# Performance work log

Hardware: AMD Instinct MI355X
Metric: run time of the kernel (lower is better)

Reference implementation:

```python
import jax, jax.numpy as jnp
import numpy as np
from jax import lax

N = 16384
K = 16
EPS = 1e-5


def setup_inputs() -> dict:
    key = jax.random.key(0)
    ks = jax.random.split(key, 10)

    def w(k, shape):
        fan_in = shape[0]
        return jax.random.normal(k, shape, jnp.float32) / np.sqrt(fan_in)

    return {
        "pos": jax.random.normal(ks[0], (N, 3), jnp.float32),
        "normal": jax.random.normal(ks[1], (N, 3), jnp.float32),
        # conv1 mlp: Linear(9,64) -> GroupNorm(8,64) -> ReLU -> Linear(64,64)
        "W1a": w(ks[2], (9, 64)), "b1a": jnp.zeros((64,), jnp.float32),
        "g1": jnp.ones((64,), jnp.float32), "beta1": jnp.zeros((64,), jnp.float32),
        "W1b": w(ks[3], (64, 64)), "b1b": jnp.zeros((64,), jnp.float32),
        # conv2 mlp: Linear(67,64) -> GroupNorm(8,64) -> ReLU -> Linear(64,64)
        "W2a": w(ks[4], (67, 64)), "b2a": jnp.zeros((64,), jnp.float32),
        "g2": jnp.ones((64,), jnp.float32), "beta2": jnp.zeros((64,), jnp.float32),
        "W2b": w(ks[5], (64, 64)), "b2b": jnp.zeros((64,), jnp.float32),
        # conv3 mlp: Linear(67,128) -> GroupNorm(16,128) -> ReLU -> Linear(128,128)
        "W3a": w(ks[6], (67, 128)), "b3a": jnp.zeros((128,), jnp.float32),
        "g3": jnp.ones((128,), jnp.float32), "beta3": jnp.zeros((128,), jnp.float32),
        "W3b": w(ks[7], (128, 128)), "b3b": jnp.zeros((128,), jnp.float32),
    }


def knn_graph(pos, k):
    # [N,N] squared distances; loop=True -> self is included (distance 0).
    sq = jnp.sum(pos * pos, axis=1)
    d2 = sq[:, None] + sq[None, :] - 2.0 * (pos @ pos.T)
    _, nbr = lax.top_k(-d2, k)  # [N,k] neighbor (source) indices per target node
    return nbr


def group_norm(h, gamma, beta, groups):
    # h: [N,k,C]; normalize each group of channels per edge sample.
    n, k, c = h.shape
    hg = h.reshape(n, k, groups, c // groups)
    mu = hg.mean(axis=-1, keepdims=True)
    var = hg.var(axis=-1, keepdims=True)
    hg = (hg - mu) * lax.rsqrt(var + EPS)
    return hg.reshape(n, k, c) * gamma + beta


def pointnet_conv(x, pos, nbr, Wa, ba, gamma, beta, Wb, bb, groups):
    # message: concat(x_j, pos_j - pos_i), MLP per edge, max-aggregate over neighbors
    xj = x[nbr]                              # [N,k,C_in]
    rel = pos[nbr] - pos[:, None, :]         # [N,k,3]
    m = jnp.concatenate([xj, rel], axis=-1)  # [N,k,C_in+3]
    h = m @ Wa + ba
    h = jax.nn.relu(group_norm(h, gamma, beta, groups))
    h = h @ Wb + bb
    return jnp.max(h, axis=1)                # [N,C_out]


def reference(pos, normal, W1a, b1a, g1, beta1, W1b, b1b,
              W2a, b2a, g2, beta2, W2b, b2b,
              W3a, b3a, g3, beta3, W3b, b3b):
    nbr = knn_graph(pos, K)
    h = jnp.concatenate([pos, normal], axis=-1)  # [N,6]
    h1 = jax.nn.relu(pointnet_conv(h, pos, nbr, W1a, b1a, g1, beta1, W1b, b1b, 8))
    h2 = jax.nn.relu(pointnet_conv(h1, pos, nbr, W2a, b2a, g2, beta2, W2b, b2b, 8))
    h3 = jax.nn.relu(pointnet_conv(h2, pos, nbr, W3a, b3a, g3, beta3, W3b, b3b, 16))
    return (h1, h2, h3)
```

## Files before the change

### kernel.cpp

```cpp
#include <hip/hip_runtime.h>
#include <hip/hip_bf16.h>
#include <stdint.h>

typedef unsigned long long u64;
typedef unsigned int u32;
typedef __attribute__((ext_vector_type(8))) short bf16x8;
typedef __attribute__((ext_vector_type(8))) unsigned short u16x8;
typedef __attribute__((ext_vector_type(4))) float f32x4;

__device__ __forceinline__ float ldv(const void* p, size_t idx, int mode) {
  return mode ? __bfloat162float(((const __hip_bfloat16*)p)[idx])
              : ((const float*)p)[idx];
}
__device__ __forceinline__ void stv(void* p, size_t idx, int mode, float v) {
  if (mode) ((__hip_bfloat16*)p)[idx] = __float2bfloat16(v);
  else      ((float*)p)[idx] = v;
}
__device__ __forceinline__ unsigned short f2bfb(float f) {
  u32 u = __float_as_uint(f);
  u32 r = u + 0x7fffu + ((u >> 16) & 1u);
  return (unsigned short)(r >> 16);
}
__device__ __forceinline__ float bfb2f(unsigned short b) {
  return __uint_as_float((u32)b << 16);
}
__device__ __forceinline__ u64 shfl64(u64 v, int src) {
  int lo = __shfl((int)(u32)(v & 0xffffffffu), src, 64);
  int hi = __shfl((int)(u32)(v >> 32), src, 64);
  return ((u64)(u32)hi << 32) | (u32)lo;
}
__device__ __forceinline__ u64 shflxor64(u64 v, int m) {
  int lo = __shfl_xor((int)(u32)(v & 0xffffffffu), m, 64);
  int hi = __shfl_xor((int)(u32)(v >> 32), m, 64);
  return ((u64)(u32)hi << 32) | (u32)lo;
}
__device__ __forceinline__ u64 shfl64w16(u64 v, int src) {
  int lo = __shfl((int)(u32)(v & 0xffffffffu), src, 16);
  int hi = __shfl((int)(u32)(v >> 32), src, 16);
  return ((u64)(u32)hi << 32) | (u32)lo;
}

__device__ __forceinline__ u32 benc(float f) {
  u32 u = __float_as_uint(f);
  return (u & 0x80000000u) ? ~u : (u | 0x80000000u);
}
__device__ __forceinline__ float bdec(u32 k) {
  return (k & 0x80000000u) ? __uint_as_float(k ^ 0x80000000u)
                           : __uint_as_float(~k);
}

__global__ void PointNetSimple_61409442398998_kernel() {}

struct CvtEnt { const void* src; float* dst; int n; };
struct CvtArgs { CvtEnt e[12]; };
struct WEnt { const void* src; unsigned short* dst; int K, N, Kpad; };
struct WArgs { WEnt e[6]; };

#define GR 32
#define GR3 (GR*GR*GR)

__global__ void setup_kernel(const void* __restrict__ pos,
                             const void* __restrict__ nrm,
                             WArgs wa, CvtArgs ca,
                             int* __restrict__ flag,
                             float4* __restrict__ pos4,
                             float* __restrict__ h0,
                             int* __restrict__ counts, int n) {
  const unsigned short* u16p = (const unsigned short*)pos;
  int cnt = 0;
  for (int k = 0; k < 32; ++k) {
    int e = (u16p[k] >> 7) & 0xff;
    if (e >= 110 && e <= 140) cnt++;
  }
  const int mode = (cnt >= 26) ? 1 : 0;

  const int nprep = n >> 8;
  const int b = blockIdx.x;
  if (b < nprep) {
    int i = b * 256 + threadIdx.x;
    float x = ldv(pos, 3*(size_t)i+0, mode);
    float y = ldv(pos, 3*(size_t)i+1, mode);
    float z = ldv(pos, 3*(size_t)i+2, mode);
    pos4[i] = make_float4(x, y, z, x*x + y*y + z*z);
    h0[6*(size_t)i+0] = x; h0[6*(size_t)i+1] = y; h0[6*(size_t)i+2] = z;
    h0[6*(size_t)i+3] = ldv(nrm, 3*(size_t)i+0, mode);
    h0[6*(size_t)i+4] = ldv(nrm, 3*(size_t)i+1, mode);
    h0[6*(size_t)i+5] = ldv(nrm, 3*(size_t)i+2, mode);
    float bmn[3] = {x, y, z}, bmx[3] = {x, y, z};
#pragma unroll
    for (int m = 32; m; m >>= 1) {
#pragma unroll
      for (int k = 0; k < 3; ++k) {
        bmn[k] = fminf(bmn[k], __shfl_xor(bmn[k], m, 64));
        bmx[k] = fmaxf(bmx[k], __shfl_xor(bmx[k], m, 64));
      }
    }
    if ((threadIdx.x & 63) == 0) {
      u32* bb = (u32*)flag;
#pragma unroll
      for (int k = 0; k < 3; ++k) {
        atomicMin(&bb[4 + k], benc(bmn[k]));
        atomicMin(&bb[7 + k], benc(-bmx[k]));
      }
    }
  } else {
    int r = b - nprep;
    if (r < 6) {
      WEnt ent = wa.e[r];
      for (int t = threadIdx.x; t < ent.N * ent.Kpad; t += blockDim.x) {
        int nn = t / ent.Kpad;
        int k  = t - nn * ent.Kpad;
        float v = (k < ent.K) ? ldv(ent.src, (size_t)k * ent.N + nn, mode) : 0.0f;
        ent.dst[t] = f2bfb(v);
      }
      if (r == 0 && threadIdx.x == 0) flag[0] = mode;
    } else if (r == 6) {
      for (int t2 = 0; t2 < 12; ++t2) {
        CvtEnt ent = ca.e[t2];
        for (int t = threadIdx.x; t < ent.n; t += blockDim.x)
          ent.dst[t] = ldv(ent.src, t, mode);
      }
    } else {
      counts[(r - 7) * 256 + threadIdx.x] = 0;
    }
  }
}

template<int CAP>
__device__ __forceinline__ void knn_flush(u64* __restrict__ wbuf, int& cnt,
                                          u64& val, u64& t15, float& th,
                                          int lane) {
  u64 cand = (lane < cnt) ? wbuf[lane] : ~0ull;
#pragma unroll
  for (int k = 2; k <= CAP; k <<= 1) {
#pragma unroll
    for (int j = k >> 1; j > 0; j >>= 1) {
      u64 other = shflxor64(cand, j);
      bool up    = ((lane & k) == 0) || (k == CAP);
      bool lower = ((lane & j) == 0);
      bool keepMin = (up == lower);
      u64 mn = cand < other ? cand : other;
      u64 mx = cand < other ? other : cand;
      cand = keepMin ? mn : mx;
    }
  }
  u64 rev = shfl64w16(cand, 15 - (lane & 15));
  u64 lo = val < rev ? val : rev;
#pragma unroll
  for (int j = 8; j > 0; j >>= 1) {
    u64 other = shflxor64(lo, j);
    bool lower = ((lane & j) == 0);
    u64 mn = lo < other ? lo : other;
    u64 mx = lo < other ? other : lo;
    lo = lower ? mn : mx;
  }
  val = (lane < 16) ? lo : ~0ull;
  t15 = shfl64(val, 15);
  u32 thb = (u32)(t15 >> 32);
  th = (thb == 0xffffffffu) ? 3.4e38f : __uint_as_float(thb);
  cnt = 0;
}

__global__ __launch_bounds__(256) void hist_kernel(
    const float4* __restrict__ pos4, const u32* __restrict__ bbx,
    int* __restrict__ counts, int* __restrict__ cid, int n) {
  const int i = blockIdx.x * 256 + threadIdx.x;
  if (i >= n) return;
  const float mnx = bdec(bbx[0]), mny = bdec(bbx[1]), mnz = bdec(bbx[2]);
  const float ihx = (float)GR / fmaxf(-bdec(bbx[3]) - mnx, 1e-20f);
  const float ihy = (float)GR / fmaxf(-bdec(bbx[4]) - mny, 1e-20f);
  const float ihz = (float)GR / fmaxf(-bdec(bbx[5]) - mnz, 1e-20f);
  float4 p = pos4[i];
  int cx = min(GR - 1, max(0, (int)((p.x - mnx) * ihx)));
  int cy = min(GR - 1, max(0, (int)((p.y - mny) * ihy)));
  int cz = min(GR - 1, max(0, (int)((p.z - mnz) * ihz)));
  int lin = (cz * GR + cy) * GR + cx;
  cid[i] = lin;
  atomicAdd(&counts[lin], 1);
}

__global__ __launch_bounds__(1024) void scan_kernel(
    const int* __restrict__ counts, int* __restrict__ cellstart,
    int* __restrict__ cursor) {
  __shared__ int part[1024];
  const int t = threadIdx.x;
  int4 v[8];
  int s = 0;
#pragma unroll
  for (int k = 0; k < 8; ++k) {
    v[k] = ((const int4*)counts)[t*8 + k];
    s += v[k].x + v[k].y + v[k].z + v[k].w;
  }
  part[t] = s;
  __syncthreads();
  for (int d = 1; d < 1024; d <<= 1) {
    int x = (t >= d) ? part[t - d] : 0;
    __syncthreads();
    part[t] += x;
    __syncthreads();
  }
  int o = part[t] - s;
#pragma unroll
  for (int k = 0; k < 8; ++k) {
    int4 c;
    c.x = o; o += v[k].x;
    c.y = o; o += v[k].y;
    c.z = o; o += v[k].z;
    c.w = o; o += v[k].w;
    ((int4*)cellstart)[t*8 + k] = c;
    ((int4*)cursor)[t*8 + k] = c;
  }
  if (t == 1023) { cellstart[GR3] = o; cursor[GR3] = o; }
}

__global__ __launch_bounds__(256) void scatter_kernel(
    const float4* __restrict__ pos4, const int* __restrict__ cid,
    int* __restrict__ cursor, int* __restrict__ sidx,
    float4* __restrict__ spos4, int n) {
  const int i = blockIdx.x * 256 + threadIdx.x;
  if (i >= n) return;
  int dst = atomicAdd(&cursor[cid[i]], 1);
  spos4[dst] = pos4[i];
  sidx[dst]  = i;
}

#define KNN7_WPB 4
__global__ __launch_bounds__(256) void knn7_kernel(
    const float4* __restrict__ spos4,
    const int* __restrict__ sidx, const int* __restrict__ cellstart,
    const u32* __restrict__ bbx, int* __restrict__ nbr, int n) {
  __shared__ u64 buf[KNN7_WPB][72];
  const int tid = threadIdx.x, lane = tid & 63, w = tid >> 6;
  const int g = blockIdx.x * KNN7_WPB + w;
  u64* wbuf = &buf[w][0];
  const float4 pi = spos4[g];
  const int target = sidx[g];

  const float mnx = bdec(bbx[0]), mny = bdec(bbx[1]), mnz = bdec(bbx[2]);
  const float ex = fmaxf(-bdec(bbx[3]) - mnx, 1e-20f);
  const float ey = fmaxf(-bdec(bbx[4]) - mny, 1e-20f);
  const float ez = fmaxf(-bdec(bbx[5]) - mnz, 1e-20f);
  const float ihx = (float)GR / ex, ihy = (float)GR / ey, ihz = (float)GR / ez;
  const float hxf = ex * (1.0f / GR), hyf = ey * (1.0f / GR), hzf = ez * (1.0f / GR);
  const int cx = min(GR - 1, max(0, (int)((pi.x - mnx) * ihx)));
  const int cy = min(GR - 1, max(0, (int)((pi.y - mny) * ihy)));
  const int cz = min(GR - 1, max(0, (int)((pi.z - mnz) * ihz)));

  u64 val = ~0ull, t15 = ~0ull;
  float th = 3.4e38f;
  int cnt = 0;
  int myseen = 0;

  auto doFlush = [&]() {
    if (cnt <= 32) knn_flush<32>(wbuf, cnt, val, t15, th, lane);
    else           knn_flush<64>(wbuf, cnt, val, t15, th, lane);
  };

  auto procSeg = [&](int p0, int p1) {
#pragma unroll 2
    for (int t0 = p0; t0 < p1; t0 += 64) {
      int gi = t0 + lane;
      bool in = gi < p1;
      float4 a = spos4[in ? gi : (p1 - 1)];
      float d2 = (pi.w + a.w) - 2.0f*(pi.x*a.x + pi.y*a.y + pi.z*a.z);
      d2 = fmaxf(d2, 0.0f);
      bool pass = in && (d2 <= th);
      u64 bal = __ballot(pass);
      if (bal) {
        int pc = __popcll(bal);
        if (cnt + pc > 64) doFlush();
        u32 mb = __builtin_amdgcn_mbcnt_lo((u32)bal, 0u);
        mb = __builtin_amdgcn_mbcnt_hi((u32)(bal >> 32), mb);
        if (pass)
          wbuf[cnt + mb] = ((u64)__float_as_uint(d2) << 32) | (u32)sidx[gi];
        cnt += pc;
      }
    }
  };

  {
    const int oc = (cz * GR + cy) * GR + cx;
    const int oLo = cellstart[oc], oHi = cellstart[oc + 1];
    if (lane == 0) myseen += oHi - oLo;
    procSeg(oLo, oHi);
    if (cnt > 0) doFlush();
  }

  for (int r = 1; r < GR; ++r) {
    const int x0 = max(cx - r, 0), x1 = min(cx + r, GR - 1);
    const int d1 = 2*r + 1, d2i = 2*r - 1;
    const int nA = 2 * d1;
    const int nB = 2 * d2i;
    const int nC = 2 * d2i * d2i;
    const int S = nA + nB + nC;
    const u32 magic = 0xFFFFFFFFu / (u32)d2i + 1u;

    for (int b0 = 0; b0 < S; b0 += 64) {
      const int s = b0 + lane;
      int zc = 0, yc = 0, xa = 0, xb = -1;
      bool live = s < S;
      if (live) {
        if (s < nA) {
          int za = s >= d1;
          int dy = s - (za ? d1 : 0) - r;
          zc = cz + (za ? r : -r); yc = cy + dy; xa = x0; xb = x1;
        } else if (s < nA + nB) {
          int t = s - nA;
          int side = t >= d2i;
          int dz = t - (side ? d2i : 0) - (r - 1);
          zc = cz + dz; yc = cy + (side ? r : -r); xa = x0; xb = x1;
        } else {
          int t = s - nA - nB;
          int side = t & 1; t >>= 1;
          int dzi = (int)__umulhi((u32)t, magic);
          int dyi = t - dzi * d2i;
          zc = cz - r + 1 + dzi; yc = cy - r + 1 + dyi;
          int xcell = side ? cx + r : cx - r;
          xa = xcell; xb = xcell;
          live = ((unsigned)xcell < GR);
        }
        live = live && ((unsigned)zc < GR) && ((unsigned)yc < GR);
      }
      int lo = 0, hi = 0;
      if (live) {
        int base = (zc * GR + yc) * GR;
        lo = cellstart[base + xa];
        hi = cellstart[base + xb + 1];
        myseen += hi - lo;
      }
      u64 bal = __ballot(live && (hi > lo));
      while (bal) {
        int l = __builtin_ctzll(bal); bal &= bal - 1;
        int p0 = __shfl(lo, l, 64), p1 = __shfl(hi, l, 64);
        procSeg(p0, p1);
      }
    }

    int tot = myseen;
#pragma unroll
    for (int m = 32; m; m >>= 1) tot += __shfl_xor(tot, m, 64);
    if (tot >= n) break;
    float mind = 3.4e38f;
    if (cx - r > 0)      mind = fminf(mind, pi.x - (mnx + (float)(cx - r) * hxf));
    if (cx + r < GR - 1) mind = fminf(mind, (mnx + (float)(cx + r + 1) * hxf) - pi.x);
    if (cy - r > 0)      mind = fminf(mind, pi.y - (mny + (float)(cy - r) * hyf));
    if (cy + r < GR - 1) mind = fminf(mind, (mny + (float)(cy + r + 1) * hyf) - pi.y);
    if (cz - r > 0)      mind = fminf(mind, pi.z - (mnz + (float)(cz - r) * hzf));
    if (cz + r < GR - 1) mind = fminf(mind, (mnz + (float)(cz + r + 1) * hzf) - pi.z);
    float mind2 = mind * mind * 0.9999f - 1e-6f;
    if (mind2 > th) break;
    if (cnt > 0) {
      doFlush();
      if (mind2 > th) break;
    }
  }
  if (cnt > 0) doFlush();
  if (lane < 16) nbr[(size_t)target * 16 + lane] = (int)(val & 0xffffffffu);
}

template<int CIN, int CMID, int KT1, int NT, int KT2>
__global__ __launch_bounds__(256, 4) void conv_mfma7_kernel(
    const float* __restrict__ xf,
    const unsigned short* __restrict__ xb,
    const float4* __restrict__ pos4,
    const int* __restrict__ nbr,
    const int* __restrict__ flag,
    const unsigned short* __restrict__ WaT,
    const unsigned short* __restrict__ WbT,
    const float* __restrict__ baf,
    const float* __restrict__ gmf,
    const float* __restrict__ btf,
    const float* __restrict__ bbf,
    unsigned short* __restrict__ xoutb,
    void* __restrict__ bout, size_t out_off)
{
  constexpr int K1PAD = KT1 * 32;
  constexpr int SB = CMID + 8;

  __shared__ unsigned short msgB[128 * SB];

  const int tid  = threadIdx.x;
  const int lane = tid & 63;
  const int w    = tid >> 6;
  const int quad = lane >> 4;
  const int cl   = lane & 15;
  const int node0 = blockIdx.x * 8;
  const int mode = flag[0];

  bf16x8 afr[2][KT1];
#pragma unroll
  for (int mt = 0; mt < 2; ++mt) {
    const int node = node0 + w*2 + mt;
    const int j = nbr[(size_t)node*16 + cl];
    const float4 pin = pos4[node];
    const float4 pj = pos4[j];
    const float rx = pj.x - pin.x, ry = pj.y - pin.y, rz = pj.z - pin.z;
    if constexpr (CIN == 64) {
#pragma unroll
      for (int kt = 0; kt < 2; ++kt)
        afr[mt][kt] = *(const bf16x8*)&xb[(size_t)j*64 + kt*32 + quad*8];
      unsigned short o[8] = {0,0,0,0,0,0,0,0};
      if (quad == 0) { o[0] = f2bfb(rx); o[1] = f2bfb(ry); o[2] = f2bfb(rz); }
      afr[mt][KT1-1] = *(bf16x8*)o;
    } else {
      unsigned short o[8] = {0,0,0,0,0,0,0,0};
      if (quad == 0) {
        const float* p = &xf[(size_t)j*6];
        o[0] = f2bfb(p[0]); o[1] = f2bfb(p[1]); o[2] = f2bfb(p[2]);
        o[3] = f2bfb(p[3]); o[4] = f2bfb(p[4]); o[5] = f2bfb(p[5]);
        o[6] = f2bfb(rx);   o[7] = f2bfb(ry);
      } else if (quad == 1) {
        o[0] = f2bfb(rz);
      }
      afr[mt][0] = *(bf16x8*)o;
    }
  }

  const int grow = lane >> 1, ggl = lane & 1;
  bf16x8 w1c[KT1], w1n[KT1];
#pragma unroll
  for (int kt = 0; kt < KT1; ++kt)
    w1c[kt] = *(const bf16x8*)&WaT[(size_t)cl * K1PAD + kt*32 + quad*8];
#pragma unroll
  for (int nt = 0; nt < NT; ++nt) {
    if (nt + 1 < NT) {
#pragma unroll
      for (int kt = 0; kt < KT1; ++kt)
        w1n[kt] = *(const bf16x8*)&WaT[(size_t)((nt+1)*16 + cl) * K1PAD + kt*32 + quad*8];
    }
    f32x4 a1[2];
    a1[0] = (f32x4){0.f, 0.f, 0.f, 0.f};
    a1[1] = (f32x4){0.f, 0.f, 0.f, 0.f};
#pragma unroll
    for (int kt = 0; kt < KT1; ++kt) {
      a1[0] = __builtin_amdgcn_mfma_f32_16x16x32_bf16(afr[0][kt], w1c[kt], a1[0], 0, 0, 0);
      a1[1] = __builtin_amdgcn_mfma_f32_16x16x32_bf16(afr[1][kt], w1c[kt], a1[1], 0, 0, 0);
    }
    float bac = baf[nt*16 + cl];
#pragma unroll
    for (int mt = 0; mt < 2; ++mt)
#pragma unroll
      for (int reg = 0; reg < 4; ++reg)
        msgB[(w*32 + mt*16 + quad*4 + reg) * SB + nt*16 + cl] =
            f2bfb(a1[mt][reg] + bac);
    asm volatile("" ::: "memory");
    {
      const int cb = nt*16 + ggl*8;
      unsigned short* p = &msgB[(w*32 + grow) * SB + cb];
      u16x8 hv = *(const u16x8*)p;
      float vv[8];
#pragma unroll
      for (int e = 0; e < 8; ++e) vv[e] = bfb2f(hv[e]);
      float s = 0.f, q = 0.f;
#pragma unroll
      for (int e = 0; e < 8; ++e) { s += vv[e]; q += vv[e]*vv[e]; }
      float mu = s * 0.125f;
      float var = q * 0.125f - mu * mu;
      float inv = rsqrtf(fmaxf(var, 0.0f) + 1e-5f);
      unsigned short o[8];
#pragma unroll
      for (int e = 0; e < 8; ++e) {
        float t = (vv[e] - mu) * inv * gmf[cb+e] + btf[cb+e];
        o[e] = f2bfb(fmaxf(t, 0.0f));
      }
      *(bf16x8*)p = *(bf16x8*)o;
    }
    asm volatile("" ::: "memory");
#pragma unroll
    for (int kt = 0; kt < KT1; ++kt) w1c[kt] = w1n[kt];
  }

  bf16x8 af0[KT2], af1[KT2];
#pragma unroll
  for (int kt = 0; kt < KT2; ++kt) {
    af0[kt] = *(const bf16x8*)&msgB[(w*32 + cl)      * SB + kt*32 + quad*8];
    af1[kt] = *(const bf16x8*)&msgB[(w*32 + 16 + cl) * SB + kt*32 + quad*8];
  }
  bf16x8 w2c[KT2], w2n[KT2];
#pragma unroll
  for (int kt = 0; kt < KT2; ++kt)
    w2c[kt] = *(const bf16x8*)&WbT[(size_t)cl * CMID + kt*32 + quad*8];
#pragma unroll
  for (int nt = 0; nt < NT; ++nt) {
    if (nt + 1 < NT) {
#pragma unroll
      for (int kt = 0; kt < KT2; ++kt)
        w2n[kt] = *(const bf16x8*)&WbT[(size_t)((nt+1)*16 + cl) * CMID + kt*32 + quad*8];
    }
    f32x4 a2[2];
    a2[0] = (f32x4){0.f, 0.f, 0.f, 0.f};
    a2[1] = (f32x4){0.f, 0.f, 0.f, 0.f};
#pragma unroll
    for (int kt = 0; kt < KT2; ++kt) {
      a2[0] = __builtin_amdgcn_mfma_f32_16x16x32_bf16(af0[kt], w2c[kt], a2[0], 0, 0, 0);
      a2[1] = __builtin_amdgcn_mfma_f32_16x16x32_bf16(af1[kt], w2c[kt], a2[1], 0, 0, 0);
    }
#pragma unroll
    for (int mt = 0; mt < 2; ++mt) {
      int node = node0 + w*2 + mt;
      float m = fmaxf(fmaxf(a2[mt][0], a2[mt][1]),
                      fmaxf(a2[mt][2], a2[mt][3]));
      m = fmaxf(m, __shfl_xor(m, 16, 64));
      m = fmaxf(m, __shfl_xor(m, 32, 64));
      float v = fmaxf(m + bbf[nt*16 + cl], 0.0f);
      if (quad == 0) {
        size_t oi = (size_t)node * CMID + nt*16 + cl;
        if (xoutb) xoutb[oi] = f2bfb(v);
        stv(bout, out_off + oi, mode, v);
      }
    }
#pragma unroll
    for (int kt = 0; kt < KT2; ++kt) w2c[kt] = w2n[kt];
  }
}

extern "C" void kernel_launch(void* const* d_in, const int* in_sizes, int n_in,
                              void* d_out, int out_size, void* d_ws, size_t ws_size,
                              hipStream_t stream) {
  (void)n_in; (void)ws_size; (void)in_sizes;
  int n = out_size / 256;
  if (n <= 0 || (n & 255)) n = 16384;

  float* ws = (float*)d_ws;
  int*    flag    = (int*)ws;
  float4* pos4    = (float4*)(ws + 16);
  float*  h0      = ws + 16 + (size_t)4*n;
  int*    nbr     = (int*)(ws + 16 + (size_t)10*n);
  unsigned short* h1b = (unsigned short*)(ws + 16 + (size_t)26*n);
  unsigned short* h2b = (unsigned short*)(ws + 16 + (size_t)58*n);
  float*  vbuf    = ws + 16 + (size_t)90*n;
  unsigned short* wtbuf = (unsigned short*)(vbuf + 1024);

  float* gbase = vbuf + 1024 + 22528;
  int*    cid       = (int*)gbase;
  int*    counts    = cid + n;
  int*    cellstart = counts + GR3;
  int*    cursor    = cellstart + 32772;
  int*    sidx      = cursor + 32772;
  float4* spos4     = (float4*)(sidx + n);

  const int vsz[12] = {64,64,64,64, 64,64,64,64, 128,128,128,128};
  const int vsrc[12] = {3,4,5,7, 9,10,11,13, 15,16,17,19};
  CvtArgs ca;
  float* vptr[12];
  {
    int off = 0;
    for (int t = 0; t < 12; ++t) {
      ca.e[t].src = d_in[vsrc[t]];
      ca.e[t].dst = vbuf + off;
      ca.e[t].n   = vsz[t];
      vptr[t] = vbuf + off;
      off += vsz[t];
    }
  }
  const int wK[6]    = {9, 64, 67, 64, 67, 128};
  const int wN[6]    = {64, 64, 64, 64, 128, 128};
  const int wKp[6]   = {32, 64, 96, 64, 96, 128};
  const int wsrc[6]  = {2, 6, 8, 12, 14, 18};
  WArgs wa;
  unsigned short* wptr[6];
  {
    int off = 0;
    for (int t = 0; t < 6; ++t) {
      wa.e[t].src  = d_in[wsrc[t]];
      wa.e[t].dst  = wtbuf + off;
      wa.e[t].K    = wK[t];
      wa.e[t].N    = wN[t];
      wa.e[t].Kpad = wKp[t];
      wptr[t] = wtbuf + off;
      off += wN[t] * wKp[t];
    }
  }

  u32* bbx = (u32*)ws + 4;
  hipMemsetAsync(bbx, 0xFF, 24, stream);

  setup_kernel<<<n/256 + 7 + GR3/256, 256, 0, stream>>>(
      d_in[0], d_in[1], wa, ca, flag, pos4, h0, counts, n);

  hist_kernel<<<n/256, 256, 0, stream>>>(pos4, bbx, counts, cid, n);
  scan_kernel<<<1, 1024, 0, stream>>>(counts, cellstart, cursor);
  scatter_kernel<<<n/256, 256, 0, stream>>>(pos4, cid, cursor, sidx, spos4, n);
  knn7_kernel<<<n/KNN7_WPB, 256, 0, stream>>>(spos4, sidx, cellstart,
                                              bbx, nbr, n);

  conv_mfma7_kernel<6, 64, 1, 4, 2><<<n/8, 256, 0, stream>>>(
      h0, (const unsigned short*)nullptr, pos4, nbr, flag, wptr[0], wptr[1],
      vptr[0], vptr[1], vptr[2], vptr[3], h1b, d_out, (size_t)0);
  conv_mfma7_kernel<64, 64, 3, 4, 2><<<n/8, 256, 0, stream>>>(
      (const float*)nullptr, h1b, pos4, nbr, flag, wptr[2], wptr[3],
      vptr[4], vptr[5], vptr[6], vptr[7], h2b, d_out, (size_t)n*64);
  conv_mfma7_kernel<64, 128, 3, 8, 4><<<n/8, 256, 0, stream>>>(
      (const float*)nullptr, h2b, pos4, nbr, flag, wptr[4], wptr[5],
      vptr[8], vptr[9], vptr[10], vptr[11],
      (unsigned short*)nullptr, d_out, (size_t)n*128);
}
```

Before: 350.0 us.

## Process conv layers in spatially sorted order for gather locality

Points are reordered by grid cell during scatter, and a rank map converts kNN neighbor indices into sorted-space indices. The conv kernels then walk nodes in sorted order and gather neighbor features from the sorted intermediate buffers. Only the final output is scattered back to original node order through sidx. Neighbors of nearby nodes should then sit close together in memory, which improves cache hit rates for the feature gathers. In exchange, scatter copies h0, the output stores become scattered, and there is one extra indirection.

```diff
diff --git a/kernel.cpp b/kernel.cpp
--- a/kernel.cpp
+++ b/kernel.cpp
@@ -214,27 +214,34 @@
 }
 
 __global__ __launch_bounds__(256) void scatter_kernel(
-    const float4* __restrict__ pos4, const int* __restrict__ cid,
+    const float4* __restrict__ pos4, const float* __restrict__ h0,
+    const int* __restrict__ cid,
     int* __restrict__ cursor, int* __restrict__ sidx,
-    float4* __restrict__ spos4, int n) {
+    float4* __restrict__ spos4, int* __restrict__ rank,
+    float* __restrict__ h0s, int n) {
   const int i = blockIdx.x * 256 + threadIdx.x;
   if (i >= n) return;
   int dst = atomicAdd(&cursor[cid[i]], 1);
   spos4[dst] = pos4[i];
   sidx[dst]  = i;
+  rank[i]    = dst;
+  const float* s = &h0[(size_t)i * 6];
+  float* d = &h0s[(size_t)dst * 6];
+#pragma unroll
+  for (int k = 0; k < 6; ++k) d[k] = s[k];
 }
 
 #define KNN7_WPB 4
 __global__ __launch_bounds__(256) void knn7_kernel(
     const float4* __restrict__ spos4,
     const int* __restrict__ sidx, const int* __restrict__ cellstart,
-    const u32* __restrict__ bbx, int* __restrict__ nbr, int n) {
+    const u32* __restrict__ bbx, const int* __restrict__ rank,
+    int* __restrict__ nbrs, int n) {
   __shared__ u64 buf[KNN7_WPB][72];
   const int tid = threadIdx.x, lane = tid & 63, w = tid >> 6;
   const int g = blockIdx.x * KNN7_WPB + w;
   u64* wbuf = &buf[w][0];
   const float4 pi = spos4[g];
-  const int target = sidx[g];
 
   const float mnx = bdec(bbx[0]), mny = bdec(bbx[1]), mnz = bdec(bbx[2]);
   const float ex = fmaxf(-bdec(bbx[3]) - mnx, 1e-20f);
@@ -355,15 +362,17 @@
     }
   }
   if (cnt > 0) doFlush();
-  if (lane < 16) nbr[(size_t)target * 16 + lane] = (int)(val & 0xffffffffu);
+  if (lane < 16)
+    nbrs[(size_t)g * 16 + lane] = rank[(int)(val & 0xffffffffu)];
 }
 
 template<int CIN, int CMID, int KT1, int NT, int KT2>
-__global__ __launch_bounds__(256, 4) void conv_mfma7_kernel(
+__global__ __launch_bounds__(256, 4) void conv_mfma9_kernel(
     const float* __restrict__ xf,
     const unsigned short* __restrict__ xb,
-    const float4* __restrict__ pos4,
-    const int* __restrict__ nbr,
+    const float4* __restrict__ spos4,
+    const int* __restrict__ nbrs,
+    const int* __restrict__ sidx,
     const int* __restrict__ flag,
     const unsigned short* __restrict__ WaT,
     const unsigned short* __restrict__ WbT,
@@ -384,28 +393,30 @@
   const int w    = tid >> 6;
   const int quad = lane >> 4;
   const int cl   = lane & 15;
-  const int node0 = blockIdx.x * 8;
+  const int sp0  = blockIdx.x * 8;
   const int mode = flag[0];
 
+  int orig[2];
   bf16x8 afr[2][KT1];
 #pragma unroll
   for (int mt = 0; mt < 2; ++mt) {
-    const int node = node0 + w*2 + mt;
-    const int j = nbr[(size_t)node*16 + cl];
-    const float4 pin = pos4[node];
-    const float4 pj = pos4[j];
+    const int sp = sp0 + w*2 + mt;
+    orig[mt] = sidx[sp];
+    const int js = nbrs[(size_t)sp*16 + cl];
+    const float4 pin = spos4[sp];
+    const float4 pj = spos4[js];
     const float rx = pj.x - pin.x, ry = pj.y - pin.y, rz = pj.z - pin.z;
     if constexpr (CIN == 64) {
 #pragma unroll
       for (int kt = 0; kt < 2; ++kt)
-        afr[mt][kt] = *(const bf16x8*)&xb[(size_t)j*64 + kt*32 + quad*8];
+        afr[mt][kt] = *(const bf16x8*)&xb[(size_t)js*64 + kt*32 + quad*8];
       unsigned short o[8] = {0,0,0,0,0,0,0,0};
       if (quad == 0) { o[0] = f2bfb(rx); o[1] = f2bfb(ry); o[2] = f2bfb(rz); }
       afr[mt][KT1-1] = *(bf16x8*)o;
     } else {
       unsigned short o[8] = {0,0,0,0,0,0,0,0};
       if (quad == 0) {
-        const float* p = &xf[(size_t)j*6];
+        const float* p = &xf[(size_t)js*6];
         o[0] = f2bfb(p[0]); o[1] = f2bfb(p[1]); o[2] = f2bfb(p[2]);
         o[3] = f2bfb(p[3]); o[4] = f2bfb(p[4]); o[5] = f2bfb(p[5]);
         o[6] = f2bfb(rx);   o[7] = f2bfb(ry);
@@ -497,16 +508,15 @@
     }
 #pragma unroll
     for (int mt = 0; mt < 2; ++mt) {
-      int node = node0 + w*2 + mt;
+      const int sp = sp0 + w*2 + mt;
       float m = fmaxf(fmaxf(a2[mt][0], a2[mt][1]),
                       fmaxf(a2[mt][2], a2[mt][3]));
       m = fmaxf(m, __shfl_xor(m, 16, 64));
       m = fmaxf(m, __shfl_xor(m, 32, 64));
       float v = fmaxf(m + bbf[nt*16 + cl], 0.0f);
       if (quad == 0) {
-        size_t oi = (size_t)node * CMID + nt*16 + cl;
-        if (xoutb) xoutb[oi] = f2bfb(v);
-        stv(bout, out_off + oi, mode, v);
+        if (xoutb) xoutb[(size_t)sp * CMID + nt*16 + cl] = f2bfb(v);
+        stv(bout, out_off + (size_t)orig[mt] * CMID + nt*16 + cl, mode, v);
       }
     }
 #pragma unroll
@@ -525,7 +535,7 @@
   int*    flag    = (int*)ws;
   float4* pos4    = (float4*)(ws + 16);
   float*  h0      = ws + 16 + (size_t)4*n;
-  int*    nbr     = (int*)(ws + 16 + (size_t)10*n);
+  int*    nbrs    = (int*)(ws + 16 + (size_t)10*n);
   unsigned short* h1b = (unsigned short*)(ws + 16 + (size_t)26*n);
   unsigned short* h2b = (unsigned short*)(ws + 16 + (size_t)58*n);
   float*  vbuf    = ws + 16 + (size_t)90*n;
@@ -538,6 +548,8 @@
   int*    cursor    = cellstart + 32772;
   int*    sidx      = cursor + 32772;
   float4* spos4     = (float4*)(sidx + n);
+  int*    rank      = (int*)(sidx + n + 4*n);
+  float*  h0s       = (float*)(rank + n);
 
   const int vsz[12] = {64,64,64,64, 64,64,64,64, 128,128,128,128};
   const int vsrc[12] = {3,4,5,7, 9,10,11,13, 15,16,17,19};
@@ -580,18 +592,21 @@
 
   hist_kernel<<<n/256, 256, 0, stream>>>(pos4, bbx, counts, cid, n);
   scan_kernel<<<1, 1024, 0, stream>>>(counts, cellstart, cursor);
-  scatter_kernel<<<n/256, 256, 0, stream>>>(pos4, cid, cursor, sidx, spos4, n);
+  scatter_kernel<<<n/256, 256, 0, stream>>>(pos4, h0, cid, cursor, sidx,
+                                            spos4, rank, h0s, n);
   knn7_kernel<<<n/KNN7_WPB, 256, 0, stream>>>(spos4, sidx, cellstart,
-                                              bbx, nbr, n);
-
-  conv_mfma7_kernel<6, 64, 1, 4, 2><<<n/8, 256, 0, stream>>>(
-      h0, (const unsigned short*)nullptr, pos4, nbr, flag, wptr[0], wptr[1],
-      vptr[0], vptr[1], vptr[2], vptr[3], h1b, d_out, (size_t)0);
-  conv_mfma7_kernel<64, 64, 3, 4, 2><<<n/8, 256, 0, stream>>>(
-      (const float*)nullptr, h1b, pos4, nbr, flag, wptr[2], wptr[3],
-      vptr[4], vptr[5], vptr[6], vptr[7], h2b, d_out, (size_t)n*64);
-  conv_mfma7_kernel<64, 128, 3, 8, 4><<<n/8, 256, 0, stream>>>(
-      (const float*)nullptr, h2b, pos4, nbr, flag, wptr[4], wptr[5],
-      vptr[8], vptr[9], vptr[10], vptr[11],
+                                              bbx, rank, nbrs, n);
+
+  conv_mfma9_kernel<6, 64, 1, 4, 2><<<n/8, 256, 0, stream>>>(
+      h0s, (const unsigned short*)nullptr, spos4, nbrs, sidx, flag,
+      wptr[0], wptr[1], vptr[0], vptr[1], vptr[2], vptr[3],
+      h1b, d_out, (size_t)0);
+  conv_mfma9_kernel<64, 64, 3, 4, 2><<<n/8, 256, 0, stream>>>(
+      (const float*)nullptr, h1b, spos4, nbrs, sidx, flag,
+      wptr[2], wptr[3], vptr[4], vptr[5], vptr[6], vptr[7],
+      h2b, d_out, (size_t)n*64);
+  conv_mfma9_kernel<64, 128, 3, 8, 4><<<n/8, 256, 0, stream>>>(
+      (const float*)nullptr, h2b, spos4, nbrs, sidx, flag,
+      wptr[4], wptr[5], vptr[8], vptr[9], vptr[10], vptr[11],
       (unsigned short*)nullptr, d_out, (size_t)n*128);
 }
```

After: 350.2 us. About the same (+0.1%).
